# Optimization experiments

Hardware: AMD Instinct MI355X
Metric: run time of the kernel (lower is better)

Reference implementation:

```python
import jax, jax.numpy as jnp
import numpy as np

N_NODES = 100000
DEG = 16
N_EDGES = N_NODES * DEG
R = 8          # num_relations
C_IN = 64
C_OUT = 64


def setup_inputs() -> dict:
    key = jax.random.key(0)
    k1, k2, k3, k4 = jax.random.split(key, 4)
    x_feat = jax.random.normal(k1, (N_NODES, C_IN), dtype=jnp.float32)
    # xavier-ish scale for weight
    scale = (6.0 / (C_IN + C_OUT)) ** 0.5
    weight = jax.random.uniform(k2, (R + 1, C_IN, C_OUT), dtype=jnp.float32,
                                minval=-scale, maxval=scale)
    bias = jnp.zeros((C_OUT,), dtype=jnp.float32)
    # fixed-degree CSR: row_ptr = arange * DEG
    csr_row_ptr = (jnp.arange(N_NODES + 1, dtype=jnp.int64) * DEG)
    csr_col_ind = jax.random.randint(k3, (N_EDGES,), 0, N_NODES, dtype=jnp.int64)
    edge_type = jax.random.randint(k4, (N_EDGES,), 0, R, dtype=jnp.int64)
    return {"x_feat": x_feat, "weight": weight, "bias": bias,
            "csr_row_ptr": csr_row_ptr, "csr_col_ind": csr_col_ind,
            "edge_type": edge_type, "dup_count": DEG}


def reference(x_feat, weight, bias, csr_row_ptr, csr_col_ind, edge_type, dup_count):
    n_dst = csr_row_ptr.shape[0] - 1
    n_edges = csr_col_ind.shape[0]
    # per-edge destination node ids from CSR row pointer
    degrees = jnp.diff(csr_row_ptr)
    dst = jnp.repeat(jnp.arange(n_dst, dtype=csr_row_ptr.dtype), degrees,
                     total_repeat_length=n_edges)
    # segment id = (dst, relation) pair
    seg = (dst * R + edge_type).astype(jnp.int32)
    gathered = x_feat[csr_col_ind]                                  # [E, C_in]
    sums = jax.ops.segment_sum(gathered, seg, num_segments=n_dst * R)  # [N*R, C_in]
    counts = jax.ops.segment_sum(jnp.ones((n_edges,), x_feat.dtype), seg,
                                 num_segments=n_dst * R)
    # mean aggregation per (node, relation); empty relations -> 0
    agg = sums / jnp.maximum(counts, 1.0)[:, None]
    agg = agg.reshape(n_dst, R * x_feat.shape[1])                   # [N, R*C_in]
    # root (self) feature appended last, matching weight[-1]
    x_agg = jnp.concatenate([agg, x_feat[:n_dst]], axis=1)          # [N, (R+1)*C_in]
    y = x_agg @ weight.reshape(-1, weight.shape[-1]) + bias         # [N, C_out]
    return y
```

## Files before the change

kernel.cpp:

```cpp
#include <hip/hip_runtime.h>
#include <hip/hip_bf16.h>

#define R_REL   8
#define C_DIM   64
#define K_DIM   576
#define KT_N    18
#define CT_N    4
#define TILE_M  16
#define K_PAD   584
#define PACK_T  (KT_N * CT_N * 64)

typedef __attribute__((ext_vector_type(8))) short bf16x8;
typedef __attribute__((ext_vector_type(4))) float f32x4;
typedef __attribute__((ext_vector_type(2))) unsigned u32x2;


static __device__ __forceinline__ unsigned short f2bf(float f) {
    union { float f; unsigned u; } v; v.f = f;
    unsigned r = v.u + 0x7FFFu + ((v.u >> 16) & 1u);
    return (unsigned short)(r >> 16);
}
static __device__ __forceinline__ float bf2f(unsigned u16) {
    union { unsigned u; float f; } v; v.u = u16 << 16;
    return v.f;
}

__global__ void prep_kernel(const float* __restrict__ x, const float* __restrict__ wt,
                            unsigned short* __restrict__ xb, unsigned int* __restrict__ wf,
                            int total_cvt) {
    int t = blockIdx.x * 256 + threadIdx.x;
    if (t < PACK_T) {
        int lane = t & 63;
        int ct   = (t >> 6) & 3;
        int kt   = t >> 8;
        int row0 = kt * 32 + (lane >> 4) * 8;
        int col  = ct * 16 + (lane & 15);
        unsigned short v[8];
#pragma unroll
        for (int j = 0; j < 8; ++j) {
            int rk = row0 + j;
            int wr;
            if (rk < 512) {
                int rel = rk & 7, c = (rk >> 3) & 15, g = rk >> 7;
                wr = rel * C_DIM + g * 16 + c;
            } else {
                wr = 512 + ((rk - 512) & 3) * 16 + ((rk - 512) >> 2);
            }
            v[j] = f2bf(wt[wr * C_DIM + col]);
        }
        uint4 o;
        o.x = (unsigned)v[0] | ((unsigned)v[1] << 16);
        o.y = (unsigned)v[2] | ((unsigned)v[3] << 16);
        o.z = (unsigned)v[4] | ((unsigned)v[5] << 16);
        o.w = (unsigned)v[6] | ((unsigned)v[7] << 16);
        ((uint4*)wf)[t] = o;
        return;
    }
    int tc = t - PACK_T;
    if (tc >= total_cvt) return;
    int n = tc >> 4, c = tc & 15;
    const float* xr = x + (size_t)n * C_DIM + c;
    ushort4 o;
    o.x = f2bf(xr[0]);
    o.y = f2bf(xr[16]);
    o.z = f2bf(xr[32]);
    o.w = f2bf(xr[48]);
    *(ushort4*)(xb + (size_t)n * C_DIM + c * 4) = o;
}

#define ACCUM_SWITCH(RELV, VV)                                  \
    switch (RELV) {                                             \
        case 0: s0 += (VV); ++c0; break;                        \
        case 1: s1 += (VV); ++c1; break;                        \
        case 2: s2 += (VV); ++c2; break;                        \
        case 3: s3 += (VV); ++c3; break;                        \
        case 4: s4 += (VV); ++c4; break;                        \
        case 5: s5 += (VV); ++c5; break;                        \
        case 6: s6 += (VV); ++c6; break;                        \
        default: s7 += (VV); ++c7; break;                       \
    }

template<int USE_BF>
__global__ __launch_bounds__(256, 8) void rgcn_kernel(
    const float* __restrict__ x_feat,
    const unsigned short* __restrict__ xb,
    const float* __restrict__ bias,
    const int*   __restrict__ row_ptr,
    const int*   __restrict__ col_ind,
    const int*   __restrict__ edge_type,
    const unsigned short* __restrict__ wfrag,
    float* __restrict__ out,
    int n_nodes)
{
    __shared__ __align__(16) unsigned short xa[TILE_M][K_PAD];
    __shared__ __align__(8)  unsigned char  rel_lds[4][64];
    __shared__ __align__(4)  unsigned short inv_lds[4][32];

    const int tid   = threadIdx.x;
    const int lane  = tid & 63;
    const int w     = tid >> 6;
    const int m0    = blockIdx.x * TILE_M;
    const int nbase = m0 + w * 4;

    const int n_l   = nbase + (lane >> 4);
    const bool v_l  = n_l < n_nodes;
    int rp0   = v_l ? row_ptr[n_l]     : 0;
    int rp1   = v_l ? row_ptr[n_l + 1] : 0;
    int deg_l = v_l ? (rp1 - rp0) : -1;
    int col_l = col_ind[rp0 + (lane & 15)];
    int rel_l = edge_type[rp0 + (lane & 15)];

    const bool fast = USE_BF && (__ballot(deg_l == 16) == ~0ull);

    if (fast) {
        rel_lds[w][lane] = (unsigned char)rel_l;
        unsigned long long bsel = 0;
#pragma unroll
        for (int r = 0; r < 8; ++r) {
            unsigned long long b = __ballot(rel_l == r);
            bsel = ((lane & 7) == r) ? b : bsel;
        }
        if (lane < 32) {
            int nd  = (lane >> 3) & 3;
            int cnt = __popcll(bsel & (0xFFFFull << (nd * 16)));
            inv_lds[w][lane] = f2bf(1.0f / (float)(cnt > 0 ? cnt : 1));
        }

        u32x2 selfv = *(const u32x2*)(xb + (size_t)(nbase + (lane >> 4)) * C_DIM
                                      + (lane & 15) * 4);
        *(u32x2*)&xa[w * 4 + (lane >> 4)][8 * C_DIM + (lane & 15) * 4] = selfv;

        const int q   = lane >> 4;
        const int q8b = q << 5;
        int src0[8], src1[8];
#pragma unroll
        for (int e = 0; e < 8; ++e) {
            src0[e] = __builtin_amdgcn_ds_bpermute(q8b + e * 4,       col_l);
            src1[e] = __builtin_amdgcn_ds_bpermute(q8b + 128 + e * 4, col_l);
        }

        const unsigned short* xbase = xb + (lane & 15) * 4;
        u32x2 gv0[8], gv1[8];
#pragma unroll
        for (int e = 0; e < 8; ++e) {
            gv0[e] = *(const u32x2*)(xbase + (size_t)src0[e] * C_DIM);
            gv1[e] = *(const u32x2*)(xbase + (size_t)src1[e] * C_DIM);
        }

        unsigned bw0[4][4], bw1[4][4];
#pragma unroll
        for (int d = 0; d < 4; ++d) {
            unsigned lx = gv0[2*d].x, hx = gv0[2*d+1].x;
            unsigned ly = gv0[2*d].y, hy = gv0[2*d+1].y;
            bw0[0][d] = (lx & 0xFFFFu) | (hx << 16);
            bw0[1][d] = (lx >> 16)     | (hx & 0xFFFF0000u);
            bw0[2][d] = (ly & 0xFFFFu) | (hy << 16);
            bw0[3][d] = (ly >> 16)     | (hy & 0xFFFF0000u);
            lx = gv1[2*d].x; hx = gv1[2*d+1].x;
            ly = gv1[2*d].y; hy = gv1[2*d+1].y;
            bw1[0][d] = (lx & 0xFFFFu) | (hx << 16);
            bw1[1][d] = (lx >> 16)     | (hx & 0xFFFF0000u);
            bw1[2][d] = (ly & 0xFFFFu) | (hy << 16);
            bw1[3][d] = (ly >> 16)     | (hy & 0xFFFF0000u);
        }

        const unsigned rl    = lane & 7;
        const bool     hi_ok = (lane >> 5) == ((lane & 15) >> 3);
        const int rb   = (q & 1) * 4;
        const int nrow = q >> 1;
#pragma unroll
        for (int pr = 0; pr < 2; ++pr) {
            const unsigned char* relp = &rel_lds[w][pr * 32 + q * 8];
            unsigned rlo = *(const unsigned*)relp;
            unsigned rhi = *(const unsigned*)(relp + 4);
            unsigned inv16 = inv_lds[w][(pr * 2 + ((lane & 15) >> 3)) * 8 + (lane & 7)];
            unsigned invg  = hi_ok ? inv16 : 0u;
            unsigned af[4];
#pragma unroll
            for (int d = 0; d < 4; ++d) {
                unsigned wrd = (d < 2) ? rlo : rhi;
                unsigned b0 = (wrd >> ((d & 1) * 16)) & 0xFFu;
                unsigned b1 = (wrd >> ((d & 1) * 16 + 8)) & 0xFFu;
                af[d] = (b0 == rl ? invg : 0u) | ((b1 == rl ? invg : 0u) << 16);
            }
            union { unsigned u[4]; bf16x8 v; } au;
            au.u[0] = af[0]; au.u[1] = af[1]; au.u[2] = af[2]; au.u[3] = af[3];

            unsigned short* xrow = &xa[w * 4 + pr * 2 + nrow][(lane & 15) * 8 + rb];
#pragma unroll
            for (int g = 0; g < 4; ++g) {
                union { unsigned u[4]; bf16x8 v; } bu;
                if (pr == 0) {
                    bu.u[0] = bw0[g][0]; bu.u[1] = bw0[g][1];
                    bu.u[2] = bw0[g][2]; bu.u[3] = bw0[g][3];
                } else {
                    bu.u[0] = bw1[g][0]; bu.u[1] = bw1[g][1];
                    bu.u[2] = bw1[g][2]; bu.u[3] = bw1[g][3];
                }
                f32x4 dacc = __builtin_amdgcn_mfma_f32_16x16x32_bf16(
                                 au.v, bu.v, (f32x4){0.f, 0.f, 0.f, 0.f}, 0, 0, 0);
                unsigned w0p = (unsigned)f2bf(dacc[0]) | ((unsigned)f2bf(dacc[1]) << 16);
                unsigned w1p = (unsigned)f2bf(dacc[2]) | ((unsigned)f2bf(dacc[3]) << 16);
                *(unsigned*)(xrow + g * 128)     = w0p;
                *(unsigned*)(xrow + g * 128 + 2) = w1p;
            }
        }
    } else {
        for (int mi_ = 0; mi_ < 4; ++mi_) {
            const int mi = w * 4 + mi_;
            const int n  = nbase + mi_;
            const int sdeg  = __builtin_amdgcn_readlane(deg_l, mi_ * 16);
            const int sbase = __builtin_amdgcn_readlane(rp0,   mi_ * 16);
            if (sdeg < 0) {
                for (int k = lane; k < K_DIM; k += 64) xa[mi][k] = 0;
                continue;
            }
            float s0=0,s1=0,s2=0,s3=0,s4=0,s5=0,s6=0,s7=0;
            int   c0=0,c1=0,c2=0,c3=0,c4=0,c5=0,c6=0,c7=0;
            const int ich = (lane & 15) * 4 + (lane >> 4);
            for (int e = 0; e < sdeg; ++e) {
                int src = col_ind[sbase + e];
                int rlv = edge_type[sbase + e];
                float vv = USE_BF ? bf2f(xb[(size_t)src * C_DIM + ich])
                                  : x_feat[(size_t)src * C_DIM + lane];
                ACCUM_SWITCH(rlv, vv)
            }
            const int kb = (lane >> 4) * 128 + (lane & 15) * 8;
            xa[mi][kb + 0] = f2bf(s0 * __fdividef(1.0f, (float)(c0>0?c0:1)));
            xa[mi][kb + 1] = f2bf(s1 * __fdividef(1.0f, (float)(c1>0?c1:1)));
            xa[mi][kb + 2] = f2bf(s2 * __fdividef(1.0f, (float)(c2>0?c2:1)));
            xa[mi][kb + 3] = f2bf(s3 * __fdividef(1.0f, (float)(c3>0?c3:1)));
            xa[mi][kb + 4] = f2bf(s4 * __fdividef(1.0f, (float)(c4>0?c4:1)));
            xa[mi][kb + 5] = f2bf(s5 * __fdividef(1.0f, (float)(c5>0?c5:1)));
            xa[mi][kb + 6] = f2bf(s6 * __fdividef(1.0f, (float)(c6>0?c6:1)));
            xa[mi][kb + 7] = f2bf(s7 * __fdividef(1.0f, (float)(c7>0?c7:1)));
            xa[mi][8*C_DIM+lane] = USE_BF ? (unsigned short)xb[(size_t)n * C_DIM + lane]
                                          : f2bf(x_feat[(size_t)n * C_DIM
                                                        + (lane & 3) * 16 + (lane >> 2)]);
        }
    }
    __syncthreads();

    const int ct   = w;
    f32x4 acc = {0,0,0,0};
    const int arow = lane & 15;
    const int kgrp2 = lane >> 4;
    const bf16x8* wf8 = (const bf16x8*)wfrag;
#pragma unroll
    for (int kt = 0; kt < KT_N; ++kt) {
        bf16x8 a = *(const bf16x8*)&xa[arow][kt * 32 + kgrp2 * 8];
        acc = __builtin_amdgcn_mfma_f32_16x16x32_bf16(a, wf8[(kt*4 + ct)*64 + lane], acc, 0,0,0);
    }

    const int col   = ct * 16 + (lane & 15);
    const float b   = bias[col];
    const int rbase = (lane >> 4) * 4;
#pragma unroll
    for (int j = 0; j < 4; ++j) {
        int n = m0 + rbase + j;
        if (n < n_nodes)
            out[n * C_DIM + col] = acc[j] + b;
    }
}

extern "C" void kernel_launch(void* const* d_in, const int* in_sizes, int n_in,
                              void* d_out, int out_size, void* d_ws, size_t ws_size,
                              hipStream_t stream) {
    const float* x_feat    = (const float*)d_in[0];
    const float* weight    = (const float*)d_in[1];
    const float* bias      = (const float*)d_in[2];
    const int*   row_ptr   = (const int*)d_in[3];
    const int*   col_ind   = (const int*)d_in[4];
    const int*   edge_type = (const int*)d_in[5];
    float* out = (float*)d_out;

    const int n_nodes = in_sizes[3] - 1;
    const int nblocks = (n_nodes + TILE_M - 1) / TILE_M;

    unsigned int* wfrag = (unsigned int*)d_ws;
    const size_t wf_bytes = (size_t)PACK_T * 16;
    const size_t xb_bytes = (size_t)n_nodes * C_DIM * 2;

    if (ws_size >= wf_bytes + xb_bytes) {
        unsigned short* xb = (unsigned short*)((char*)d_ws + wf_bytes);
        int total_cvt = n_nodes * 16;
        int prep_blocks = (PACK_T + total_cvt + 255) / 256;
        prep_kernel<<<prep_blocks, 256, 0, stream>>>(x_feat, weight, xb, wfrag, total_cvt);
        rgcn_kernel<1><<<nblocks, 256, 0, stream>>>(x_feat, xb, bias, row_ptr, col_ind,
                                                    edge_type, (const unsigned short*)d_ws,
                                                    out, n_nodes);
    } else {
        prep_kernel<<<(PACK_T + 255) / 256, 256, 0, stream>>>(x_feat, weight, nullptr, wfrag, 0);
        rgcn_kernel<0><<<nblocks, 256, 0, stream>>>(x_feat, nullptr, bias, row_ptr, col_ind,
                                                    edge_type, (const unsigned short*)d_ws,
                                                    out, n_nodes);
    }
}
```

Baseline: 51.67 us.

## Process two tiles per block and prefetch second tile's gathers early

Each block now handles two 16-node tiles. Metadata and neighbor-feature gathers for the second tile are issued before the first tile is finished, so memory latency overlaps with the first tile's aggregation and GEMM. This doubles the live gather registers, so launch bounds drop from 8 to 4 waves per EU, and the grid is halved. The cost is lower occupancy and extra syncthreads.

```diff
diff --git a/kernel.cpp b/kernel.cpp
--- a/kernel.cpp
+++ b/kernel.cpp
@@ -81,7 +81,7 @@
     }
 
 template<int USE_BF>
-__global__ __launch_bounds__(256, 8) void rgcn_kernel(
+__global__ __launch_bounds__(256, 4) void rgcn_kernel(
     const float* __restrict__ x_feat,
     const unsigned short* __restrict__ xb,
     const float* __restrict__ bias,
@@ -99,25 +99,39 @@
     const int tid   = threadIdx.x;
     const int lane  = tid & 63;
     const int w     = tid >> 6;
-    const int m0    = blockIdx.x * TILE_M;
-    const int nbase = m0 + w * 4;
-
-    const int n_l   = nbase + (lane >> 4);
-    const bool v_l  = n_l < n_nodes;
-    int rp0   = v_l ? row_ptr[n_l]     : 0;
-    int rp1   = v_l ? row_ptr[n_l + 1] : 0;
-    int deg_l = v_l ? (rp1 - rp0) : -1;
-    int col_l = col_ind[rp0 + (lane & 15)];
-    int rel_l = edge_type[rp0 + (lane & 15)];
-
-    const bool fast = USE_BF && (__ballot(deg_l == 16) == ~0ull);
-
-    if (fast) {
-        rel_lds[w][lane] = (unsigned char)rel_l;
+    const int ntiles = (n_nodes + TILE_M - 1) / TILE_M;
+
+    auto META = [&](int tile, int& rp0v, int& degv, int& colv, int& relv) {
+        int nl = tile * TILE_M + w * 4 + (lane >> 4);
+        bool vl = nl < n_nodes;
+        rp0v = vl ? row_ptr[nl] : 0;
+        int rp1v = vl ? row_ptr[nl + 1] : 0;
+        degv = vl ? (rp1v - rp0v) : -1;
+        colv = col_ind[rp0v + (lane & 15)];
+        relv = edge_type[rp0v + (lane & 15)];
+    };
+
+    auto GISSUE = [&](int tile, int colv, u32x2 (&g0)[8], u32x2 (&g1)[8], u32x2& sv) {
+        const int q8b = (lane >> 4) << 5;
+        const unsigned short* xbase = xb + (lane & 15) * 4;
+#pragma unroll
+        for (int e = 0; e < 8; ++e) {
+            int s0 = __builtin_amdgcn_ds_bpermute(q8b + e * 4,       colv);
+            int s1 = __builtin_amdgcn_ds_bpermute(q8b + 128 + e * 4, colv);
+            g0[e] = *(const u32x2*)(xbase + (size_t)s0 * C_DIM);
+            g1[e] = *(const u32x2*)(xbase + (size_t)s1 * C_DIM);
+        }
+        int sn = tile * TILE_M + w * 4 + (lane >> 4);
+        if (sn >= n_nodes) sn = 0;
+        sv = *(const u32x2*)(xb + (size_t)sn * C_DIM + (lane & 15) * 4);
+    };
+
+    auto FIN = [&](int relv, u32x2 (&g0)[8], u32x2 (&g1)[8], u32x2 sv) {
+        rel_lds[w][lane] = (unsigned char)relv;
         unsigned long long bsel = 0;
 #pragma unroll
         for (int r = 0; r < 8; ++r) {
-            unsigned long long b = __ballot(rel_l == r);
+            unsigned long long b = __ballot(relv == r);
             bsel = ((lane & 7) == r) ? b : bsel;
         }
         if (lane < 32) {
@@ -125,45 +139,26 @@
             int cnt = __popcll(bsel & (0xFFFFull << (nd * 16)));
             inv_lds[w][lane] = f2bf(1.0f / (float)(cnt > 0 ? cnt : 1));
         }
-
-        u32x2 selfv = *(const u32x2*)(xb + (size_t)(nbase + (lane >> 4)) * C_DIM
-                                      + (lane & 15) * 4);
-        *(u32x2*)&xa[w * 4 + (lane >> 4)][8 * C_DIM + (lane & 15) * 4] = selfv;
-
-        const int q   = lane >> 4;
-        const int q8b = q << 5;
-        int src0[8], src1[8];
-#pragma unroll
-        for (int e = 0; e < 8; ++e) {
-            src0[e] = __builtin_amdgcn_ds_bpermute(q8b + e * 4,       col_l);
-            src1[e] = __builtin_amdgcn_ds_bpermute(q8b + 128 + e * 4, col_l);
-        }
-
-        const unsigned short* xbase = xb + (lane & 15) * 4;
-        u32x2 gv0[8], gv1[8];
-#pragma unroll
-        for (int e = 0; e < 8; ++e) {
-            gv0[e] = *(const u32x2*)(xbase + (size_t)src0[e] * C_DIM);
-            gv1[e] = *(const u32x2*)(xbase + (size_t)src1[e] * C_DIM);
-        }
+        *(u32x2*)&xa[w * 4 + (lane >> 4)][8 * C_DIM + (lane & 15) * 4] = sv;
 
         unsigned bw0[4][4], bw1[4][4];
 #pragma unroll
         for (int d = 0; d < 4; ++d) {
-            unsigned lx = gv0[2*d].x, hx = gv0[2*d+1].x;
-            unsigned ly = gv0[2*d].y, hy = gv0[2*d+1].y;
+            unsigned lx = g0[2*d].x, hx = g0[2*d+1].x;
+            unsigned ly = g0[2*d].y, hy = g0[2*d+1].y;
             bw0[0][d] = (lx & 0xFFFFu) | (hx << 16);
             bw0[1][d] = (lx >> 16)     | (hx & 0xFFFF0000u);
             bw0[2][d] = (ly & 0xFFFFu) | (hy << 16);
             bw0[3][d] = (ly >> 16)     | (hy & 0xFFFF0000u);
-            lx = gv1[2*d].x; hx = gv1[2*d+1].x;
-            ly = gv1[2*d].y; hy = gv1[2*d+1].y;
+            lx = g1[2*d].x; hx = g1[2*d+1].x;
+            ly = g1[2*d].y; hy = g1[2*d+1].y;
             bw1[0][d] = (lx & 0xFFFFu) | (hx << 16);
             bw1[1][d] = (lx >> 16)     | (hx & 0xFFFF0000u);
             bw1[2][d] = (ly & 0xFFFFu) | (hy << 16);
             bw1[3][d] = (ly >> 16)     | (hy & 0xFFFF0000u);
         }
 
+        const int q = lane >> 4;
         const unsigned rl    = lane & 7;
         const bool     hi_ok = (lane >> 5) == ((lane & 15) >> 3);
         const int rb   = (q & 1) * 4;
@@ -205,12 +200,14 @@
                 *(unsigned*)(xrow + g * 128 + 2) = w1p;
             }
         }
-    } else {
+    };
+
+    auto GENERAL = [&](int tile, int rp0v, int degv) {
         for (int mi_ = 0; mi_ < 4; ++mi_) {
             const int mi = w * 4 + mi_;
-            const int n  = nbase + mi_;
-            const int sdeg  = __builtin_amdgcn_readlane(deg_l, mi_ * 16);
-            const int sbase = __builtin_amdgcn_readlane(rp0,   mi_ * 16);
+            const int n  = tile * TILE_M + w * 4 + mi_;
+            const int sdeg  = __builtin_amdgcn_readlane(degv, mi_ * 16);
+            const int sbase = __builtin_amdgcn_readlane(rp0v, mi_ * 16);
             if (sdeg < 0) {
                 for (int k = lane; k < K_DIM; k += 64) xa[mi][k] = 0;
                 continue;
@@ -238,28 +235,63 @@
                                           : f2bf(x_feat[(size_t)n * C_DIM
                                                         + (lane & 3) * 16 + (lane >> 2)]);
         }
-    }
+    };
+
+    auto PHASE2 = [&](int tile) {
+        const int ct = w;
+        f32x4 acc = {0,0,0,0};
+        const int arow = lane & 15;
+        const int kgrp2 = lane >> 4;
+        const bf16x8* wf8 = (const bf16x8*)wfrag;
+#pragma unroll
+        for (int kt = 0; kt < KT_N; ++kt) {
+            bf16x8 a = *(const bf16x8*)&xa[arow][kt * 32 + kgrp2 * 8];
+            acc = __builtin_amdgcn_mfma_f32_16x16x32_bf16(a, wf8[(kt*4 + ct)*64 + lane],
+                                                          acc, 0,0,0);
+        }
+        const int col = ct * 16 + (lane & 15);
+        const float b = bias[col];
+        const int rbase = (lane >> 4) * 4;
+        const int mb = tile * TILE_M;
+#pragma unroll
+        for (int j = 0; j < 4; ++j) {
+            int n = mb + rbase + j;
+            if (n < n_nodes)
+                out[n * C_DIM + col] = acc[j] + b;
+        }
+    };
+
+    const int t0 = blockIdx.x * 2;
+    const int t1 = t0 + 1;
+    const bool has1 = t1 < ntiles;
+
+    int rp0a, dega, cola, rela;
+    META(t0, rp0a, dega, cola, rela);
+    const bool fast0 = USE_BF && (__ballot(dega == 16) == ~0ull);
+
+    u32x2 ga0[8], ga1[8], sva;
+    if (fast0) GISSUE(t0, cola, ga0, ga1, sva);
+
+    int rp0b = 0, degb = -1, colb = 0, relb = 0;
+    bool fast1 = false;
+    if (has1) {
+        META(t1, rp0b, degb, colb, relb);
+        fast1 = USE_BF && (__ballot(degb == 16) == ~0ull);
+    }
+    u32x2 gb0[8], gb1[8], svb;
+    if (fast1) GISSUE(t1, colb, gb0, gb1, svb);
+
+    if (fast0) FIN(rela, ga0, ga1, sva);
+    else       GENERAL(t0, rp0a, dega);
     __syncthreads();
-
-    const int ct   = w;
-    f32x4 acc = {0,0,0,0};
-    const int arow = lane & 15;
-    const int kgrp2 = lane >> 4;
-    const bf16x8* wf8 = (const bf16x8*)wfrag;
-#pragma unroll
-    for (int kt = 0; kt < KT_N; ++kt) {
-        bf16x8 a = *(const bf16x8*)&xa[arow][kt * 32 + kgrp2 * 8];
-        acc = __builtin_amdgcn_mfma_f32_16x16x32_bf16(a, wf8[(kt*4 + ct)*64 + lane], acc, 0,0,0);
-    }
-
-    const int col   = ct * 16 + (lane & 15);
-    const float b   = bias[col];
-    const int rbase = (lane >> 4) * 4;
-#pragma unroll
-    for (int j = 0; j < 4; ++j) {
-        int n = m0 + rbase + j;
-        if (n < n_nodes)
-            out[n * C_DIM + col] = acc[j] + b;
+    PHASE2(t0);
+
+    if (has1) {
+        __syncthreads();
+        if (fast1) FIN(relb, gb0, gb1, svb);
+        else       GENERAL(t1, rp0b, degb);
+        __syncthreads();
+        PHASE2(t1);
     }
 }
 
@@ -275,7 +307,8 @@
     float* out = (float*)d_out;
 
     const int n_nodes = in_sizes[3] - 1;
-    const int nblocks = (n_nodes + TILE_M - 1) / TILE_M;
+    const int ntiles  = (n_nodes + TILE_M - 1) / TILE_M;
+    const int nblocks = (ntiles + 1) / 2;
 
     unsigned int* wfrag = (unsigned int*)d_ws;
     const size_t wf_bytes = (size_t)PACK_T * 16;
```

Measured after the change: 91.41 us. 1.77x slower.
